# Optimization experiments

Hardware: AMD Instinct MI355X
Metric: run time of the kernel (lower is better)

## Reference

```python
import jax, jax.numpy as jnp
import numpy as np

B = 256
H, W = 8, 16          # input_resolution for channels=256
C = 768               # dim = channels*3
WS = 4                # window_size
SHIFT = 2             # shift_size
NH = 12               # num_heads
HD = C // NH          # head_dim = 64
HID = 1024            # mlp hidden = channels*4
N = WS * WS           # tokens per window = 16
NW = (H // WS) * (W // WS)  # windows per image = 8
LN_EPS = 1e-5


def _rel_pos_index():
    coords = np.stack(np.meshgrid(np.arange(WS), np.arange(WS), indexing='ij'))  # [2,ws,ws]
    cf = coords.reshape(2, -1)                      # [2, N]
    rel = (cf[:, :, None] - cf[:, None, :]).transpose(1, 2, 0)  # [N, N, 2]
    rel[:, :, 0] += WS - 1
    rel[:, :, 1] += WS - 1
    rel[:, :, 0] *= 2 * WS - 1
    return jnp.asarray(rel.sum(-1))                 # [N, N] int


def _attn_mask():
    img = np.zeros((H, W))
    slices = (slice(0, -WS), slice(-WS, -SHIFT), slice(-SHIFT, None))
    cnt = 0
    for hs in slices:
        for ws_ in slices:
            img[hs, ws_] = cnt
            cnt += 1
    mw = img.reshape(H // WS, WS, W // WS, WS).transpose(0, 2, 1, 3).reshape(-1, N)  # [nW, N]
    am = mw[:, None, :] - mw[:, :, None]            # [nW, N, N]
    return jnp.asarray(np.where(am != 0, -100.0, 0.0).astype(np.float32))


REL_IDX = _rel_pos_index()
ATTN_MASK = _attn_mask()


def _ln(x, g, b):
    m = x.mean(-1, keepdims=True)
    v = ((x - m) ** 2).mean(-1, keepdims=True)
    return (x - m) / jnp.sqrt(v + LN_EPS) * g + b


def setup_inputs() -> dict:
    key = jax.random.key(0)
    ks = jax.random.split(key, 8)
    s = 0.02
    return {
        'x': jax.random.normal(ks[0], (B, H * W, C), jnp.float32),
        'ln1_g': jnp.ones((C,), jnp.float32),
        'ln1_b': jnp.zeros((C,), jnp.float32),
        'qkv_w': jax.random.normal(ks[1], (C, 3 * C), jnp.float32) * s,
        'qkv_b': jnp.zeros((3 * C,), jnp.float32),
        'proj_w': jax.random.normal(ks[2], (C, C), jnp.float32) * s,
        'proj_b': jnp.zeros((C,), jnp.float32),
        'rel_table': jax.random.normal(ks[3], ((2 * WS - 1) * (2 * WS - 1), NH), jnp.float32) * s,
        'ln2_g': jnp.ones((C,), jnp.float32),
        'ln2_b': jnp.zeros((C,), jnp.float32),
        'fc1_w': jax.random.normal(ks[4], (C, HID), jnp.float32) * s,
        'fc1_b': jax.random.normal(ks[5], (HID,), jnp.float32) * 1e-6,
        'fc2_w': jax.random.normal(ks[6], (HID, C), jnp.float32) * s,
        'fc2_b': jax.random.normal(ks[7], (C,), jnp.float32) * 1e-6,
    }


def reference(x, ln1_g, ln1_b, qkv_w, qkv_b, proj_w, proj_b, rel_table,
              ln2_g, ln2_b, fc1_w, fc1_b, fc2_w, fc2_b):
    # --- norm1 + cyclic shift + window partition ---
    h = _ln(x, ln1_g, ln1_b).reshape(B, H, W, C)
    h = jnp.roll(h, (-SHIFT, -SHIFT), axis=(1, 2))
    hw = h.reshape(B, H // WS, WS, W // WS, WS, C).transpose(0, 1, 3, 2, 4, 5)
    hw = hw.reshape(B * NW, N, C)                   # (num_windows*B, N, C)
    # --- window attention with relative position bias + shift mask ---
    qkv = (hw @ qkv_w + qkv_b).reshape(B * NW, N, 3, NH, HD).transpose(2, 0, 3, 1, 4)
    q, k, v = qkv[0] * (HD ** -0.5), qkv[1], qkv[2]  # [Bn, NH, N, HD]
    attn = jnp.einsum('bhnd,bhmd->bhnm', q, k)      # [Bn, NH, N, N]
    bias = rel_table[REL_IDX].transpose(2, 0, 1)    # [NH, N, N]
    attn = attn + bias[None]
    attn = attn.reshape(B, NW, NH, N, N) + ATTN_MASK[None, :, None]
    attn = jax.nn.softmax(attn.reshape(B * NW, NH, N, N), axis=-1)
    o = jnp.einsum('bhnm,bhmd->bhnd', attn, v).transpose(0, 2, 1, 3).reshape(B * NW, N, C)
    o = o @ proj_w + proj_b
    # --- window reverse + reverse shift + residual ---
    o = o.reshape(B, H // WS, W // WS, WS, WS, C).transpose(0, 1, 3, 2, 4, 5).reshape(B, H, W, C)
    o = jnp.roll(o, (SHIFT, SHIFT), axis=(1, 2)).reshape(B, H * W, C)
    x = x + o
    # --- MLP block (dropout is identity at inference) ---
    y = _ln(x, ln2_g, ln2_b)
    y = jax.nn.gelu(y @ fc1_w + fc1_b, approximate=False)
    return x + (y @ fc2_w + fc2_b)
```

## Files before the change

kernel.cpp:

```cpp
#include <hip/hip_runtime.h>
#include <stdint.h>
#include <stddef.h>

typedef __attribute__((ext_vector_type(8))) short bf16x8;
typedef __attribute__((ext_vector_type(4))) float f32x4;
typedef __attribute__((ext_vector_type(4))) unsigned int uint4v;

static __device__ __forceinline__ unsigned short f2bf(float f) {
  unsigned int u = __builtin_bit_cast(unsigned int, f);
  unsigned int r = (u + 0x7FFFu + ((u >> 16) & 1u)) >> 16;
  return (unsigned short)r;
}

static __device__ __forceinline__ void gld16(const void* g, void* l) {
  __builtin_amdgcn_global_load_lds(
      (const __attribute__((address_space(1))) void*)g,
      (__attribute__((address_space(3))) void*)l, 16, 0, 0);
}

__global__ void transpose_cast(const float* __restrict__ src,
                               unsigned short* __restrict__ dst, int R, int C) {
  __shared__ float tile[32][33];
  int c0 = blockIdx.x * 32, r0 = blockIdx.y * 32;
  int tx = threadIdx.x, ty = threadIdx.y;
  #pragma unroll
  for (int i = 0; i < 32; i += 8)
    tile[ty + i][tx] = src[(size_t)(r0 + ty + i) * C + c0 + tx];
  __syncthreads();
  #pragma unroll
  for (int i = 0; i < 32; i += 8)
    dst[(size_t)(c0 + ty + i) * R + r0 + tx] = f2bf(tile[tx][ty + i]);
}

static __device__ __forceinline__ float blksum256(float v, float* sb) {
  #pragma unroll
  for (int o = 32; o > 0; o >>= 1) v += __shfl_down(v, o, 64);
  int lane = threadIdx.x & 63, w = threadIdx.x >> 6;
  __syncthreads();
  if (lane == 0) sb[w] = v;
  __syncthreads();
  return sb[0] + sb[1] + sb[2] + sb[3];
}

template <int MODE>
__global__ __launch_bounds__(256) void ln_kernel(const float* __restrict__ x,
                                                 const float* __restrict__ gg,
                                                 const float* __restrict__ bb,
                                                 unsigned short* __restrict__ out) {
  __shared__ float sb[4];
  const int d = blockIdx.x;
  size_t srow;
  if (MODE == 0) {
    int b = d >> 7, wid = (d >> 4) & 7, tok = d & 15;
    int oh = (((wid >> 2) << 2) + (tok >> 2) + 2) & 7;
    int ow = (((wid & 3) << 2) + (tok & 3) + 2) & 15;
    srow = (size_t)(b << 7) + oh * 16 + ow;
  } else {
    srow = d;
  }
  const float* xr = x + srow * 768;
  const int t = threadIdx.x;
  float v0 = xr[t], v1 = xr[t + 256], v2 = xr[t + 512];
  float mean = blksum256(v0 + v1 + v2, sb) * (1.0f / 768.0f);
  float d0 = v0 - mean, d1 = v1 - mean, d2 = v2 - mean;
  float var = blksum256(d0 * d0 + d1 * d1 + d2 * d2, sb) * (1.0f / 768.0f);
  float rstd = rsqrtf(var + 1e-5f);
  size_t o = (size_t)d * 768;
  out[o + t]       = f2bf(d0 * rstd * gg[t] + bb[t]);
  out[o + t + 256] = f2bf(d1 * rstd * gg[t + 256] + bb[t + 256]);
  out[o + t + 512] = f2bf(d2 * rstd * gg[t + 512] + bb[t + 512]);
}

template <int EPI>
__global__ __launch_bounds__(512, 2) void gemm256(
    const unsigned short* __restrict__ A, const unsigned short* __restrict__ BT,
    const float* __restrict__ bias, float* __restrict__ outF,
    unsigned short* __restrict__ outB, const float* __restrict__ resid,
    int M, int N, int K, int NT) {
  __shared__ __align__(16) unsigned short sA[2][256 * 64];
  __shared__ __align__(16) unsigned short sB[2][256 * 64];

  const int tid = threadIdx.x;
  const int lane = tid & 63, wv = tid >> 6;
  const int wr = wv >> 2, wc = wv & 3;
  const int fr = lane & 15, q4 = (lane >> 4) << 2;

  const int nwg = gridDim.x;
  const int orig = blockIdx.x;
  const int swz = (orig & 7) * (nwg >> 3) + (orig >> 3);
  const int mt = swz / NT, nt = swz - mt * NT;
  const int m0 = mt << 8, n0 = nt << 8;

  const size_t K2 = (size_t)K * 2;

  const int srow = tid >> 3;
  const int sg = tid & 7;
  const int sgs = ((sg ^ (srow & 7)) << 4);
  const char* pA = (const char*)A + (size_t)(m0 + srow) * K2 + sgs;
  const char* pB = (const char*)BT + (size_t)(n0 + srow) * K2 + sgs;
  char* sdA = (char*)&sA[0][0] + (wv << 10);
  char* sdB = (char*)&sB[0][0] + (wv << 10);

  const int g0 = (((lane >> 4) ^ (fr & 7)) << 4);
  const int g1 = (((4 + (lane >> 4)) ^ (fr & 7)) << 4);
  const int arow = (wr << 7) + fr;
  const int brow = (wc << 6) + fr;

  f32x4 acc[8][4];
  #pragma unroll
  for (int i = 0; i < 8; ++i)
    #pragma unroll
    for (int j = 0; j < 4; ++j) acc[i][j] = (f32x4){0.f, 0.f, 0.f, 0.f};

  bf16x8 af[4][2];
  bf16x8 bbv[2][2][2];
  const int KT = K >> 6;
  const int NI = KT >> 1;

#define BARR __builtin_amdgcn_s_barrier()
#define SCB __builtin_amdgcn_sched_barrier(0)
#define LGKM0 asm volatile("s_waitcnt lgkmcnt(0)" ::: "memory")
#define VM2 asm volatile("s_waitcnt vmcnt(2)" ::: "memory")
#define VM0 asm volatile("s_waitcnt vmcnt(0)" ::: "memory")

#define LDA(CB, mh)                                                          \
  {                                                                          \
    const char* ba = ((const char*)&sA[0][0]) + (CB)*32768;                  \
    _Pragma("unroll") for (int fm = 0; fm < 4; ++fm) {                       \
      const int r = arow + (mh)*64 + fm * 16;                                \
      af[fm][0] = *(const bf16x8*)(ba + r * 128 + g0);                       \
      af[fm][1] = *(const bf16x8*)(ba + r * 128 + g1);                       \
    }                                                                        \
  }
#define LDB(CB, nh)                                                          \
  {                                                                          \
    const char* ba = ((const char*)&sB[0][0]) + (CB)*32768;                  \
    _Pragma("unroll") for (int fn = 0; fn < 2; ++fn) {                       \
      const int r = brow + (nh)*32 + fn * 16;                                \
      bbv[nh][fn][0] = *(const bf16x8*)(ba + r * 128 + g0);                  \
      bbv[nh][fn][1] = *(const bf16x8*)(ba + r * 128 + g1);                  \
    }                                                                        \
  }
#define STG(CB, tt, j)                                                       \
  {                                                                          \
    const size_t ko = (size_t)(tt) << 7;                                     \
    gld16(pA + (size_t)((j)*64) * K2 + ko, sdA + (CB)*32768 + (j)*8192);     \
    gld16(pB + (size_t)((j)*64) * K2 + ko, sdB + (CB)*32768 + (j)*8192);     \
  }
#define MMAQ(mh, nh)                                                         \
  _Pragma("unroll") for (int fm = 0; fm < 4; ++fm)                           \
      _Pragma("unroll") for (int fn = 0; fn < 2; ++fn) {                     \
    f32x4* ac = &acc[(mh)*4 + fm][(nh)*2 + fn];                              \
    *ac = __builtin_amdgcn_mfma_f32_16x16x32_bf16(af[fm][0], bbv[nh][fn][0], \
                                                  *ac, 0, 0, 0);             \
    *ac = __builtin_amdgcn_mfma_f32_16x16x32_bf16(af[fm][1], bbv[nh][fn][1], \
                                                  *ac, 0, 0, 0);             \
  }
#define OPEN  SCB; BARR; LGKM0; SCB; __builtin_amdgcn_s_setprio(1)
#define OPEN_NOLD  SCB; BARR; __builtin_amdgcn_s_setprio(1)
#define CLOSE __builtin_amdgcn_s_setprio(0)

  #pragma unroll
  for (int j = 0; j < 4; ++j) STG(0, 0, j);
  STG(1, 1, 0);
  VM2;
  BARR;

  for (int i = 0; i < NI; ++i) {
    const int s1 = 2 * i + 1, s2 = 2 * i + 2, s3 = 2 * i + 3;
    const bool gl = (i + 1 < NI);
    LDB(0, 0) LDA(0, 0) STG(1, s1, 1)
    OPEN; MMAQ(0, 0); CLOSE; BARR;
    LDB(0, 1) STG(1, s1, 2)
    OPEN; MMAQ(0, 1); CLOSE; BARR;
    LDA(0, 1) STG(1, s1, 3)
    OPEN; MMAQ(1, 1); CLOSE; BARR;
    if (gl) STG(0, s2, 0)
    OPEN_NOLD; MMAQ(1, 0); CLOSE;
    if (gl) { VM2; } else { VM0; }
    BARR;
    LDB(1, 0) LDA(1, 0)
    if (gl) STG(0, s2, 1)
    OPEN; MMAQ(0, 0); CLOSE; BARR;
    LDB(1, 1)
    if (gl) STG(0, s2, 2)
    OPEN; MMAQ(0, 1); CLOSE; BARR;
    LDA(1, 1)
    if (gl) STG(0, s2, 3)
    OPEN; MMAQ(1, 1); CLOSE; BARR;
    if (gl) STG(1, s3, 0)
    OPEN_NOLD; MMAQ(1, 0); CLOSE;
    if (gl) { VM2; } else { VM0; }
    BARR;
  }
#undef BARR
#undef SCB
#undef LGKM0
#undef VM2
#undef VM0
#undef LDA
#undef LDB
#undef STG
#undef MMAQ
#undef OPEN
#undef OPEN_NOLD
#undef CLOSE

  #pragma unroll
  for (int ai = 0; ai < 8; ++ai) {
    #pragma unroll
    for (int bj = 0; bj < 4; ++bj) {
      const int col = n0 + (wc << 6) + bj * 16 + fr;
      const float bc = bias[col];
      #pragma unroll
      for (int i = 0; i < 4; ++i) {
        const int row = m0 + (wr << 7) + ai * 16 + q4 + i;
        float v = acc[ai][bj][i] + bc;
        if (EPI == 0) {
          outB[(size_t)row * N + col] = f2bf(v);
        } else if (EPI == 1) {
          int b = row >> 7, wid = (row >> 4) & 7, tok = row & 15;
          int oh = (((wid >> 2) << 2) + (tok >> 2) + 2) & 7;
          int ow = (((wid & 3) << 2) + (tok & 3) + 2) & 15;
          size_t di = ((size_t)(b << 7) + oh * 16 + ow) * 768 + col;
          outF[di] = v + resid[di];
        } else if (EPI == 2) {
          float g = 0.5f * v * (1.0f + erff(v * 0.70710678118f));
          outB[(size_t)row * N + col] = f2bf(g);
        } else {
          size_t di = (size_t)row * N + col;
          outF[di] = v + resid[di];
        }
      }
    }
  }
}

__global__ __launch_bounds__(64) void attn_win(const unsigned short* __restrict__ qkv,
                                               const float* __restrict__ rel_table,
                                               unsigned short* __restrict__ o) {
  __shared__ __align__(16) unsigned short q_s[16 * 64];
  __shared__ __align__(16) unsigned short k_s[16 * 64];
  __shared__ __align__(16) unsigned short vt_s[64 * 32];
  __shared__ __align__(16) unsigned short p_s[16 * 32];
  const int bid = blockIdx.x;
  const int win = bid / 12;
  const int head = bid - win * 12;
  const int wid = win & 7;
  const int lane = threadIdx.x;
  const unsigned short* gq =
      qkv + (size_t)win * 16 * 2304 + head * 64 + (size_t)(lane >> 2) * 2304 + ((lane & 3) << 4);
  const int t = lane >> 2, d0 = (lane & 3) << 4;
  *(uint4v*)&q_s[t * 64 + d0]     = *(const uint4v*)(gq);
  *(uint4v*)&q_s[t * 64 + d0 + 8] = *(const uint4v*)(gq + 8);
  *(uint4v*)&k_s[t * 64 + d0]     = *(const uint4v*)(gq + 768);
  *(uint4v*)&k_s[t * 64 + d0 + 8] = *(const uint4v*)(gq + 776);
  unsigned short vv[16];
  *(uint4v*)&vv[0] = *(const uint4v*)(gq + 1536);
  *(uint4v*)&vv[8] = *(const uint4v*)(gq + 1544);
  #pragma unroll
  for (int e = 0; e < 16; ++e) vt_s[(d0 + e) * 32 + t] = vv[e];
  #pragma unroll
  for (int e = 0; e < 16; ++e) vt_s[lane * 32 + 16 + e] = 0;
  if (lane < 16) {
    #pragma unroll
    for (int e = 0; e < 16; ++e) p_s[lane * 32 + 16 + e] = 0;
  }
  __syncthreads();

  const int fr = lane & 15, kg = (lane >> 4) << 3;
  bf16x8 qa0 = *(const bf16x8*)&q_s[fr * 64 + kg];
  bf16x8 qa1 = *(const bf16x8*)&q_s[fr * 64 + 32 + kg];
  bf16x8 ka0 = *(const bf16x8*)&k_s[fr * 64 + kg];
  bf16x8 ka1 = *(const bf16x8*)&k_s[fr * 64 + 32 + kg];
  f32x4 s = (f32x4){0.f, 0.f, 0.f, 0.f};
  s = __builtin_amdgcn_mfma_f32_16x16x32_bf16(qa0, ka0, s, 0, 0, 0);
  s = __builtin_amdgcn_mfma_f32_16x16x32_bf16(qa1, ka1, s, 0, 0, 0);

  const int wh = wid >> 2, wwc = wid & 3;
  const int rj = fr >> 2, cj = fr & 3;
  const int rowm = wh * 4 + rj, colm = wwc * 4 + cj;
  const int rgm = (rowm < 4 ? 0 : (rowm < 6 ? 1 : 2)) * 3 +
                  (colm < 12 ? 0 : (colm < 14 ? 1 : 2));
  float p[4];
  #pragma unroll
  for (int i = 0; i < 4; ++i) {
    int n = ((lane >> 4) << 2) + i;
    int ri = n >> 2, ci = n & 3;
    int rown = wh * 4 + ri, coln = wwc * 4 + ci;
    int rgn = (rown < 4 ? 0 : (rown < 6 ? 1 : 2)) * 3 +
              (coln < 12 ? 0 : (coln < 14 ? 1 : 2));
    float bias = rel_table[(size_t)((ri - rj + 3) * 7 + (ci - cj + 3)) * 12 + head];
    p[i] = s[i] * 0.125f + bias + (rgn != rgm ? -100.0f : 0.0f);
  }
  float mx[4] = {p[0], p[1], p[2], p[3]};
  #pragma unroll
  for (int off = 8; off > 0; off >>= 1)
    #pragma unroll
    for (int i = 0; i < 4; ++i) mx[i] = fmaxf(mx[i], __shfl_xor(mx[i], off, 64));
  float sm[4];
  #pragma unroll
  for (int i = 0; i < 4; ++i) { p[i] = __expf(p[i] - mx[i]); sm[i] = p[i]; }
  #pragma unroll
  for (int off = 8; off > 0; off >>= 1)
    #pragma unroll
    for (int i = 0; i < 4; ++i) sm[i] += __shfl_xor(sm[i], off, 64);
  #pragma unroll
  for (int i = 0; i < 4; ++i)
    p_s[(((lane >> 4) << 2) + i) * 32 + fr] = f2bf(p[i] / sm[i]);
  __syncthreads();

  bf16x8 pa = *(const bf16x8*)&p_s[fr * 32 + kg];
  const f32x4 oz = (f32x4){0.f, 0.f, 0.f, 0.f};
  #pragma unroll
  for (int c = 0; c < 4; ++c) {
    bf16x8 vb = *(const bf16x8*)&vt_s[(c * 16 + fr) * 32 + kg];
    f32x4 oa = __builtin_amdgcn_mfma_f32_16x16x32_bf16(pa, vb, oz, 0, 0, 0);
    #pragma unroll
    for (int i = 0; i < 4; ++i) {
      int n = ((lane >> 4) << 2) + i;
      o[((size_t)win * 16 + n) * 768 + head * 64 + c * 16 + fr] = f2bf(oa[i]);
    }
  }
}

extern "C" void kernel_launch(void* const* d_in, const int* in_sizes, int n_in,
                              void* d_out, int out_size, void* d_ws, size_t ws_size,
                              hipStream_t stream) {
  const float* x      = (const float*)d_in[0];
  const float* ln1_g  = (const float*)d_in[1];
  const float* ln1_b  = (const float*)d_in[2];
  const float* qkv_w  = (const float*)d_in[3];
  const float* qkv_b  = (const float*)d_in[4];
  const float* proj_w = (const float*)d_in[5];
  const float* proj_b = (const float*)d_in[6];
  const float* rel_t  = (const float*)d_in[7];
  const float* ln2_g  = (const float*)d_in[8];
  const float* ln2_b  = (const float*)d_in[9];
  const float* fc1_w  = (const float*)d_in[10];
  const float* fc1_b  = (const float*)d_in[11];
  const float* fc2_w  = (const float*)d_in[12];
  const float* fc2_b  = (const float*)d_in[13];
  float* out = (float*)d_out;

  char* ws = (char*)d_ws;
  unsigned short* wsA = (unsigned short*)(ws);
  unsigned short* qkvb = (unsigned short*)(ws + 50331648);
  float* xr = (float*)(ws + 50331648);
  unsigned short* h1 = (unsigned short*)(ws + 201326592);
  unsigned short* qkv_wT = (unsigned short*)(ws + 268435456);
  unsigned short* proj_wT = (unsigned short*)(ws + 271974400);
  unsigned short* fc1_wT = (unsigned short*)(ws + 273154048);
  unsigned short* fc2_wT = (unsigned short*)(ws + 274726912);

  dim3 tb(32, 8);
  transpose_cast<<<dim3(2304 / 32, 768 / 32), tb, 0, stream>>>(qkv_w, qkv_wT, 768, 2304);
  transpose_cast<<<dim3(768 / 32, 768 / 32), tb, 0, stream>>>(proj_w, proj_wT, 768, 768);
  transpose_cast<<<dim3(1024 / 32, 768 / 32), tb, 0, stream>>>(fc1_w, fc1_wT, 768, 1024);
  transpose_cast<<<dim3(768 / 32, 1024 / 32), tb, 0, stream>>>(fc2_w, fc2_wT, 1024, 768);

  ln_kernel<0><<<32768, 256, 0, stream>>>(x, ln1_g, ln1_b, wsA);
  gemm256<0><<<dim3(128 * 9), 512, 0, stream>>>(wsA, qkv_wT, qkv_b, nullptr, qkvb,
                                                nullptr, 32768, 2304, 768, 9);
  attn_win<<<24576, 64, 0, stream>>>(qkvb, rel_t, wsA);
  gemm256<1><<<dim3(128 * 3), 512, 0, stream>>>(wsA, proj_wT, proj_b, xr, nullptr,
                                                x, 32768, 768, 768, 3);
  ln_kernel<1><<<32768, 256, 0, stream>>>(xr, ln2_g, ln2_b, wsA);
  gemm256<2><<<dim3(128 * 4), 512, 0, stream>>>(wsA, fc1_wT, fc1_b, nullptr, h1,
                                                nullptr, 32768, 1024, 768, 4);
  gemm256<3><<<dim3(128 * 3), 512, 0, stream>>>(h1, fc2_wT, fc2_b, out, nullptr,
                                                xr, 32768, 768, 1024, 3);
}
```

Baseline: 580.4 us.

## Prefetch the whole next K-tile early and split the A/B global-to-LDS loads

Reworks the bf16 MFMA GEMM's global-to-LDS prefetch schedule. The prologue now stages both LDS buffers in full. Inside the loop, the A and B tile loads for the next stage are issued separately and placed right after the matching LDS regions have been read into registers. The wait threshold rises from vmcnt(2) to vmcnt(8), so more loads stay in flight and global latency overlaps more of the MFMA work. The cost is a more delicate buffer-reuse ordering that depends on the barrier placement, and more outstanding memory operations.

Measured after the change: 545.6 us. 6.0% less time.

```diff
diff --git a/kernel.cpp b/kernel.cpp
--- a/kernel.cpp
+++ b/kernel.cpp
@@ -120,7 +120,7 @@
 #define BARR __builtin_amdgcn_s_barrier()
 #define SCB __builtin_amdgcn_sched_barrier(0)
 #define LGKM0 asm volatile("s_waitcnt lgkmcnt(0)" ::: "memory")
-#define VM2 asm volatile("s_waitcnt vmcnt(2)" ::: "memory")
+#define VM8 asm volatile("s_waitcnt vmcnt(8)" ::: "memory")
 #define VM0 asm volatile("s_waitcnt vmcnt(0)" ::: "memory")
 
 #define LDA(CB, mh)                                                          \
@@ -141,12 +141,12 @@
       bbv[nh][fn][1] = *(const bf16x8*)(ba + r * 128 + g1);                  \
     }                                                                        \
   }
-#define STG(CB, tt, j)                                                       \
-  {                                                                          \
-    const size_t ko = (size_t)(tt) << 7;                                     \
-    gld16(pA + (size_t)((j)*64) * K2 + ko, sdA + (CB)*32768 + (j)*8192);     \
-    gld16(pB + (size_t)((j)*64) * K2 + ko, sdB + (CB)*32768 + (j)*8192);     \
-  }
+#define STGA(CB, tt, j)                                                      \
+  gld16(pA + (size_t)((j)*64) * K2 + ((size_t)(tt) << 7),                    \
+        sdA + (CB)*32768 + (j)*8192);
+#define STGB(CB, tt, j)                                                      \
+  gld16(pB + (size_t)((j)*64) * K2 + ((size_t)(tt) << 7),                    \
+        sdB + (CB)*32768 + (j)*8192);
 #define MMAQ(mh, nh)                                                         \
   _Pragma("unroll") for (int fm = 0; fm < 4; ++fm)                           \
       _Pragma("unroll") for (int fn = 0; fn < 2; ++fn) {                     \
@@ -161,46 +161,49 @@
 #define CLOSE __builtin_amdgcn_s_setprio(0)
 
   #pragma unroll
-  for (int j = 0; j < 4; ++j) STG(0, 0, j);
-  STG(1, 1, 0);
-  VM2;
+  for (int j = 0; j < 4; ++j) { STGA(0, 0, j); STGB(0, 0, j); }
+  #pragma unroll
+  for (int j = 0; j < 4; ++j) { STGA(1, 1, j); STGB(1, 1, j); }
+  VM8;
   BARR;
 
   for (int i = 0; i < NI; ++i) {
-    const int s1 = 2 * i + 1, s2 = 2 * i + 2, s3 = 2 * i + 3;
+    const int s2 = 2 * i + 2, s3 = 2 * i + 3;
     const bool gl = (i + 1 < NI);
-    LDB(0, 0) LDA(0, 0) STG(1, s1, 1)
+    LDB(0, 0) LDA(0, 0)
     OPEN; MMAQ(0, 0); CLOSE; BARR;
-    LDB(0, 1) STG(1, s1, 2)
+    LDB(0, 1)
+    if (gl) { STGA(0, s2, 0); STGA(0, s2, 2); }
     OPEN; MMAQ(0, 1); CLOSE; BARR;
-    LDA(0, 1) STG(1, s1, 3)
+    LDA(0, 1)
+    if (gl) { STGB(0, s2, 0); STGB(0, s2, 1); }
     OPEN; MMAQ(1, 1); CLOSE; BARR;
-    if (gl) STG(0, s2, 0)
+    if (gl) { STGA(0, s2, 1); STGA(0, s2, 3); STGB(0, s2, 2); STGB(0, s2, 3); }
     OPEN_NOLD; MMAQ(1, 0); CLOSE;
-    if (gl) { VM2; } else { VM0; }
+    if (gl) { VM8; } else { VM0; }
     BARR;
     LDB(1, 0) LDA(1, 0)
-    if (gl) STG(0, s2, 1)
     OPEN; MMAQ(0, 0); CLOSE; BARR;
     LDB(1, 1)
-    if (gl) STG(0, s2, 2)
+    if (gl) { STGA(1, s3, 0); STGA(1, s3, 2); }
     OPEN; MMAQ(0, 1); CLOSE; BARR;
     LDA(1, 1)
-    if (gl) STG(0, s2, 3)
+    if (gl) { STGB(1, s3, 0); STGB(1, s3, 1); }
     OPEN; MMAQ(1, 1); CLOSE; BARR;
-    if (gl) STG(1, s3, 0)
+    if (gl) { STGA(1, s3, 1); STGA(1, s3, 3); STGB(1, s3, 2); STGB(1, s3, 3); }
     OPEN_NOLD; MMAQ(1, 0); CLOSE;
-    if (gl) { VM2; } else { VM0; }
+    if (gl) { VM8; }
     BARR;
   }
 #undef BARR
 #undef SCB
 #undef LGKM0
-#undef VM2
+#undef VM8
 #undef VM0
 #undef LDA
 #undef LDB
-#undef STG
+#undef STGA
+#undef STGB
 #undef MMAQ
 #undef OPEN
 #undef OPEN_NOLD
```
